# Optimization experiments

Measured on AMD Instinct MI355X. Metric: run time of the kernel, lower is better.

## Reference

```python
import jax, jax.numpy as jnp
import numpy as np

B, T, D, R = 16, 4096, 512, 256

def setup_inputs() -> dict:
    key = jax.random.key(0)
    z = jax.random.normal(key, (B, T, D), dtype=jnp.float32)
    # init values from the module: gegenbauer_weights = [3,0,0], temporal_alpha = -10.0
    gegenbauer_weights = jnp.array([3.0, 0.0, 0.0], dtype=jnp.float32)
    temporal_alpha = jnp.array(-10.0, dtype=jnp.float32)
    # uniformly spaced landmarks, truncated to int like torch.linspace(...).long()
    landmarks = jnp.asarray(np.linspace(0, T - 1, R).astype(np.int64))
    return {"z": z, "gegenbauer_weights": gegenbauer_weights, "temporal_alpha": temporal_alpha, "landmarks": landmarks}

def reference(z, gegenbauer_weights, temporal_alpha, landmarks):
    Bz, Tz, d = z.shape
    # F.normalize(z, dim=-1) with eps=1e-12
    norm = jnp.linalg.norm(z, axis=-1, keepdims=True)
    Q = z / jnp.maximum(norm, 1e-12)
    K = Q[:, landmarks, :]                                   # [B, R, d]
    C = jnp.einsum('btd,brd->btr', Q, K)                     # [B, T, R]
    positions = jnp.arange(Tz)[:, None]                      # [T, 1]
    lm = landmarks[None, :]                                  # [1, R]
    causal_mask = (lm < positions).astype(z.dtype)           # [T, R]
    C_masked = C * causal_mask[None, :, :]
    # Gegenbauer mixture
    alpha = jax.nn.softmax(gegenbauer_weights)
    P1 = (1.0 + C_masked) * 0.5
    P2 = (3.0 * C_masked * C_masked - 1.0) * 0.5
    P3 = (5.0 * C_masked * C_masked * C_masked - 3.0 * C_masked) * 0.5
    Phi = alpha[0] * P1 + alpha[1] * P2 + alpha[2] * P3
    # temporal decay
    temporal_dist = jnp.clip((positions.astype(z.dtype) - lm.astype(z.dtype)) / Tz, 0.0, None)  # [T, R]
    alpha_td = jax.nn.softplus(temporal_alpha)
    Phi = Phi * jnp.exp(-alpha_td * temporal_dist)[None, :, :]
    # rowsum normalize
    row_sum = jnp.maximum(Phi.sum(axis=-1, keepdims=True), 1e-6)
    Phi = Phi / row_sum
    # append constant-1 basis column
    ones = jnp.ones((Bz, Tz, 1), dtype=z.dtype)
    return jnp.concatenate([Phi, ones], axis=-1)             # [B, T, R+1]
```

## Files before the change

kernel.cpp:

```cpp
#include <hip/hip_runtime.h>


typedef float f32x4 __attribute__((ext_vector_type(4)));
typedef short s16x8 __attribute__((ext_vector_type(8)));
typedef unsigned short u16x4 __attribute__((ext_vector_type(4)));
typedef unsigned short u16x8 __attribute__((ext_vector_type(8)));

__device__ __forceinline__ unsigned short f2bf(float f) {
    unsigned u = __builtin_bit_cast(unsigned, f);
    return (unsigned short)((u + 0x7FFFu + ((u >> 16) & 1u)) >> 16);
}

__device__ __forceinline__ int load_lm(const void* lms_raw, int idx) {
    const int* l32 = (const int*)lms_raw;
    if (l32[1] == 0) {
        const long long* l64 = (const long long*)lms_raw;
        return (int)l64[idx];
    }
    return l32[idx];
}

__device__ __forceinline__ void scalars(const float* gw, const float* ta,
                                        float& a0, float& a1, float& a2, float& atd) {
    float w0 = gw[0], w1 = gw[1], w2 = gw[2];
    float wm = fmaxf(w0, fmaxf(w1, w2));
    float e0 = __expf(w0 - wm), e1 = __expf(w1 - wm), e2 = __expf(w2 - wm);
    float einv = 1.0f / (e0 + e1 + e2);
    a0 = e0 * einv; a1 = e1 * einv; a2 = e2 * einv;
    float tv = ta[0];
    atd = (tv > 0.0f) ? (tv + log1pf(__expf(-tv))) : log1pf(__expf(tv));
}

__global__ void build_kt(const float* __restrict__ z,
                         const void* __restrict__ lms_raw,
                         unsigned char* __restrict__ kb) {
    const int b = blockIdx.x >> 8;
    const int r = blockIdx.x & 255;
    const int L = threadIdx.x;
    const int lm = load_lm(lms_raw, r);

    const f32x4* zrow = (const f32x4*)(z + ((size_t)b * 4096 + (size_t)lm) * 512);
    f32x4 v0 = zrow[L * 2 + 0];
    f32x4 v1 = zrow[L * 2 + 1];
    float ss = v0.x*v0.x + v0.y*v0.y + v0.z*v0.z + v0.w*v0.w
             + v1.x*v1.x + v1.y*v1.y + v1.z*v1.z + v1.w*v1.w;
    #pragma unroll
    for (int off = 32; off >= 1; off >>= 1) ss += __shfl_xor(ss, off, 64);
    float inv = 1.0f / fmaxf(sqrtf(ss), 1e-12f);

    u16x8 o;
    o[0]=f2bf(v0.x*inv); o[1]=f2bf(v0.y*inv); o[2]=f2bf(v0.z*inv); o[3]=f2bf(v0.w*inv);
    o[4]=f2bf(v1.x*inv); o[5]=f2bf(v1.y*inv); o[6]=f2bf(v1.z*inv); o[7]=f2bf(v1.w*inv);

    const int w  = r >> 6;
    const int nf = (r >> 4) & 3;
    const int c  = r & 15;
    const int ks = L >> 2;
    const int g  = L & 3;
    size_t off = (size_t)b * 262144 + (size_t)w * 65536
               + (size_t)(ks * 4 + nf) * 1024 + (size_t)(c * 4 + g) * 16;
    *(u16x8*)(kb + off) = o;
}

__global__ __launch_bounds__(256, 4) void nystrom_mfma(const float* __restrict__ z,
                                                       const float* __restrict__ gw,
                                                       const float* __restrict__ ta,
                                                       const void* __restrict__ lms_raw,
                                                       const unsigned char* __restrict__ kb,
                                                       float* __restrict__ out) {
    __shared__ unsigned char qtile[32 * 512 * 2];
    __shared__ float s_invn[32];
    __shared__ float s_rs[4][32];
    __shared__ float s_rsi[32];

    const int tid  = threadIdx.x;
    const int lane = tid & 63;
    const int w    = tid >> 6;
    const int b    = blockIdx.x >> 7;
    const int t0   = (blockIdx.x & 127) * 32;

    const int c = lane & 15;
    const int g = lane >> 4;

    float sa0, sa1, sa2, alpha_td;
    scalars(gw, ta, sa0, sa1, sa2, alpha_td);
    const float C0 = 0.5f * (sa0 - sa1);

    const unsigned char* kbw = kb + (size_t)b * 262144 + (size_t)w * 65536
                             + (size_t)(c * 4 + g) * 16;

    u16x8 bbuf[3][4];
    #pragma unroll
    for (int p = 0; p < 2; ++p)
        #pragma unroll
        for (int nf = 0; nf < 4; ++nf)
            bbuf[p][nf] = *(const u16x8*)(kbw + (p * 4 + nf) * 1024);

    {
        const int row = tid >> 3, part = tid & 7;
        const f32x4* zr = (const f32x4*)(z + ((size_t)b * 4096 + (size_t)(t0 + row)) * 512);
        f32x4 v[16];
        #pragma unroll
        for (int i = 0; i < 16; ++i) v[i] = zr[part + 8 * i];
        float ss = 0.0f;
        #pragma unroll
        for (int i = 0; i < 16; ++i) {
            f32x4 vv = v[i];
            ss += vv.x*vv.x + vv.y*vv.y + vv.z*vv.z + vv.w*vv.w;
            u16x4 h; h[0]=f2bf(vv.x); h[1]=f2bf(vv.y); h[2]=f2bf(vv.z); h[3]=f2bf(vv.w);
            int within = ((part + 8 * i) * 8) ^ ((row & 7) << 4);
            *(u16x4*)(qtile + row * 1024 + within) = h;
        }
        ss += __shfl_xor(ss, 1, 64);
        ss += __shfl_xor(ss, 2, 64);
        ss += __shfl_xor(ss, 4, 64);
        if (part == 0) s_invn[row] = 1.0f / fmaxf(sqrtf(ss), 1e-12f);
    }
    __syncthreads();

    f32x4 acc[2][4];
    #pragma unroll
    for (int tf = 0; tf < 2; ++tf)
        #pragma unroll
        for (int nf = 0; nf < 4; ++nf)
            acc[tf][nf] = 0.0f;

    const int swz = (c & 7) << 4;
    s16x8 abuf[2][2];
    {
        int kw = (0 * 64 + g * 16) ^ swz;
        abuf[0][0] = *(const s16x8*)(qtile + c * 1024 + kw);
        abuf[0][1] = *(const s16x8*)(qtile + (c + 16) * 1024 + kw);
    }

    #pragma unroll
    for (int ks = 0; ks < 16; ++ks) {
        if (ks + 2 < 16) {
            #pragma unroll
            for (int nf = 0; nf < 4; ++nf)
                bbuf[(ks + 2) % 3][nf] =
                    *(const u16x8*)(kbw + ((ks + 2) * 4 + nf) * 1024);
        }
        if (ks + 1 < 16) {
            int kw = ((ks + 1) * 64 + g * 16) ^ swz;
            abuf[(ks + 1) & 1][0] = *(const s16x8*)(qtile + c * 1024 + kw);
            abuf[(ks + 1) & 1][1] = *(const s16x8*)(qtile + (c + 16) * 1024 + kw);
        }
        const s16x8 a0f = abuf[ks & 1][0];
        const s16x8 a1f = abuf[ks & 1][1];
        const s16x8 b0f = __builtin_bit_cast(s16x8, bbuf[ks % 3][0]);
        const s16x8 b1f = __builtin_bit_cast(s16x8, bbuf[ks % 3][1]);
        const s16x8 b2f = __builtin_bit_cast(s16x8, bbuf[ks % 3][2]);
        const s16x8 b3f = __builtin_bit_cast(s16x8, bbuf[ks % 3][3]);
        acc[0][0] = __builtin_amdgcn_mfma_f32_16x16x32_bf16(a0f, b0f, acc[0][0], 0, 0, 0);
        acc[0][1] = __builtin_amdgcn_mfma_f32_16x16x32_bf16(a0f, b1f, acc[0][1], 0, 0, 0);
        acc[0][2] = __builtin_amdgcn_mfma_f32_16x16x32_bf16(a0f, b2f, acc[0][2], 0, 0, 0);
        acc[0][3] = __builtin_amdgcn_mfma_f32_16x16x32_bf16(a0f, b3f, acc[0][3], 0, 0, 0);
        acc[1][0] = __builtin_amdgcn_mfma_f32_16x16x32_bf16(a1f, b0f, acc[1][0], 0, 0, 0);
        acc[1][1] = __builtin_amdgcn_mfma_f32_16x16x32_bf16(a1f, b1f, acc[1][1], 0, 0, 0);
        acc[1][2] = __builtin_amdgcn_mfma_f32_16x16x32_bf16(a1f, b2f, acc[1][2], 0, 0, 0);
        acc[1][3] = __builtin_amdgcn_mfma_f32_16x16x32_bf16(a1f, b3f, acc[1][3], 0, 0, 0);
    }

    int   lmv[4];
    float elm[4];
    #pragma unroll
    for (int nf = 0; nf < 4; ++nf) {
        int rr  = w * 64 + nf * 16 + c;
        lmv[nf] = load_lm(lms_raw, rr);
        elm[nf] = __expf(alpha_td * (float)lmv[nf] * (1.0f / 4096.0f));
    }
    float invn[2][4], et[2][4];
    #pragma unroll
    for (int tf = 0; tf < 2; ++tf)
        #pragma unroll
        for (int q = 0; q < 4; ++q) {
            int tl = tf * 16 + g * 4 + q;
            invn[tf][q] = s_invn[tl];
            et[tf][q]   = __expf(-alpha_td * (float)(t0 + tl) * (1.0f / 4096.0f));
        }

    float phi[2][4][4];
    float rsum[2][4];
    #pragma unroll
    for (int tf = 0; tf < 2; ++tf) {
        #pragma unroll
        for (int q = 0; q < 4; ++q) {
            int tg = t0 + tf * 16 + g * 4 + q;
            float s = 0.0f;
            #pragma unroll
            for (int nf = 0; nf < 4; ++nf) {
                float v = acc[tf][nf][q] * invn[tf][q];
                float p;
                if (lmv[nf] < tg) {
                    float c2 = v * v;
                    float p1 = fmaf(0.5f, v, 0.5f);
                    float p2 = fmaf(1.5f, c2, -0.5f);
                    float p3 = v * fmaf(2.5f, c2, -1.5f);
                    p = (sa0 * p1 + sa1 * p2 + sa2 * p3) * (et[tf][q] * elm[nf]);
                } else {
                    p = C0;
                }
                phi[tf][nf][q] = p;
                s += p;
            }
            rsum[tf][q] = s;
        }
    }

    #pragma unroll
    for (int tf = 0; tf < 2; ++tf)
        #pragma unroll
        for (int q = 0; q < 4; ++q) {
            float s = rsum[tf][q];
            s += __shfl_xor(s, 1, 64);
            s += __shfl_xor(s, 2, 64);
            s += __shfl_xor(s, 4, 64);
            s += __shfl_xor(s, 8, 64);
            rsum[tf][q] = s;
        }
    if (c == 0) {
        #pragma unroll
        for (int tf = 0; tf < 2; ++tf)
            #pragma unroll
            for (int q = 0; q < 4; ++q)
                s_rs[w][tf * 16 + g * 4 + q] = rsum[tf][q];
    }
    __syncthreads();
    if (tid < 32) {
        float s = s_rs[0][tid] + s_rs[1][tid] + s_rs[2][tid] + s_rs[3][tid];
        s_rsi[tid] = 1.0f / fmaxf(s, 1e-6f);
    }
    __syncthreads();

    #pragma unroll
    for (int tf = 0; tf < 2; ++tf)
        #pragma unroll
        for (int q = 0; q < 4; ++q) {
            int tl = tf * 16 + g * 4 + q;
            float ri = s_rsi[tl];
            size_t obase = ((size_t)b * 4096 + (size_t)(t0 + tl)) * 257
                         + (size_t)(w * 64 + c);
            #pragma unroll
            for (int nf = 0; nf < 4; ++nf)
                out[obase + nf * 16] = phi[tf][nf][q] * ri;
        }
    if (tid < 32)
        out[((size_t)b * 4096 + (size_t)(t0 + tid)) * 257 + 256] = 1.0f;
}

extern "C" void kernel_launch(void* const* d_in, const int* in_sizes, int n_in,
                              void* d_out, int out_size, void* d_ws, size_t ws_size,
                              hipStream_t stream) {
    const float* z   = (const float*)d_in[0];
    const float* gw  = (const float*)d_in[1];
    const float* ta  = (const float*)d_in[2];
    const void*  lms = (const void*)d_in[3];
    float* out = (float*)d_out;
    unsigned char* kb = (unsigned char*)d_ws;

    build_kt<<<16 * 256, 64, 0, stream>>>(z, lms, kb);
    nystrom_mfma<<<16 * 128, 256, 0, stream>>>(z, gw, ta, lms, kb, out);
}
```

Before: 68.41 us.

## Enlarge workgroup to 64 rows with 8 waves, retile MFMA and remap blocks

Each workgroup now handles 64 time rows with 512 threads. Each of the 8 waves computes a 64x32 landmark slice instead of a 32x64 one, so the per-wave global reads of the landmark matrix are halved and the Q tile in LDS is reused more. The landmark buffer layout is changed to match, the B-operand prefetch gets one more stage, and the block index is permuted to group work across XCDs. In exchange it uses more LDS per block, which may lower occupancy, and the grid has fewer, larger blocks.

```diff
diff --git a/kernel.cpp b/kernel.cpp
--- a/kernel.cpp
+++ b/kernel.cpp
@@ -52,32 +52,33 @@
     o[0]=f2bf(v0.x*inv); o[1]=f2bf(v0.y*inv); o[2]=f2bf(v0.z*inv); o[3]=f2bf(v0.w*inv);
     o[4]=f2bf(v1.x*inv); o[5]=f2bf(v1.y*inv); o[6]=f2bf(v1.z*inv); o[7]=f2bf(v1.w*inv);
 
-    const int w  = r >> 6;
-    const int nf = (r >> 4) & 3;
+    const int rt = r >> 4;
     const int c  = r & 15;
     const int ks = L >> 2;
     const int g  = L & 3;
-    size_t off = (size_t)b * 262144 + (size_t)w * 65536
-               + (size_t)(ks * 4 + nf) * 1024 + (size_t)(c * 4 + g) * 16;
+    size_t off = (size_t)b * 262144
+               + (size_t)(ks * 16 + rt) * 1024 + (size_t)(c * 4 + g) * 16;
     *(u16x8*)(kb + off) = o;
 }
 
-__global__ __launch_bounds__(256, 4) void nystrom_mfma(const float* __restrict__ z,
+__global__ __launch_bounds__(512, 4) void nystrom_mfma(const float* __restrict__ z,
                                                        const float* __restrict__ gw,
                                                        const float* __restrict__ ta,
                                                        const void* __restrict__ lms_raw,
                                                        const unsigned char* __restrict__ kb,
                                                        float* __restrict__ out) {
-    __shared__ unsigned char qtile[32 * 512 * 2];
-    __shared__ float s_invn[32];
-    __shared__ float s_rs[4][32];
-    __shared__ float s_rsi[32];
+    __shared__ unsigned char qtile[64 * 512 * 2];
+    __shared__ float s_invn[64];
+    __shared__ float s_rs[8][64];
+    __shared__ float s_rsi[64];
 
     const int tid  = threadIdx.x;
     const int lane = tid & 63;
     const int w    = tid >> 6;
-    const int b    = blockIdx.x >> 7;
-    const int t0   = (blockIdx.x & 127) * 32;
+
+    const int wgid = (blockIdx.x & 7) * 128 + (blockIdx.x >> 3);
+    const int b    = wgid >> 6;
+    const int t0   = (wgid & 63) * 64;
 
     const int c = lane & 15;
     const int g = lane >> 4;
@@ -86,15 +87,15 @@
     scalars(gw, ta, sa0, sa1, sa2, alpha_td);
     const float C0 = 0.5f * (sa0 - sa1);
 
-    const unsigned char* kbw = kb + (size_t)b * 262144 + (size_t)w * 65536
-                             + (size_t)(c * 4 + g) * 16;
-
-    u16x8 bbuf[3][4];
-    #pragma unroll
-    for (int p = 0; p < 2; ++p)
-        #pragma unroll
-        for (int nf = 0; nf < 4; ++nf)
-            bbuf[p][nf] = *(const u16x8*)(kbw + (p * 4 + nf) * 1024);
+    const unsigned char* kbw = kb + (size_t)b * 262144 + (size_t)(c * 4 + g) * 16;
+    const int rt0 = 2 * w;
+
+    u16x8 bbuf[4][2];
+    #pragma unroll
+    for (int p = 0; p < 3; ++p)
+        #pragma unroll
+        for (int nf = 0; nf < 2; ++nf)
+            bbuf[p][nf] = *(const u16x8*)(kbw + (size_t)(p * 16 + rt0 + nf) * 1024);
 
     {
         const int row = tid >> 3, part = tid & 7;
@@ -118,61 +119,58 @@
     }
     __syncthreads();
 
-    f32x4 acc[2][4];
-    #pragma unroll
-    for (int tf = 0; tf < 2; ++tf)
-        #pragma unroll
-        for (int nf = 0; nf < 4; ++nf)
+    f32x4 acc[4][2];
+    #pragma unroll
+    for (int tf = 0; tf < 4; ++tf)
+        #pragma unroll
+        for (int nf = 0; nf < 2; ++nf)
             acc[tf][nf] = 0.0f;
 
     const int swz = (c & 7) << 4;
-    s16x8 abuf[2][2];
+    s16x8 abuf[2][4];
     {
         int kw = (0 * 64 + g * 16) ^ swz;
-        abuf[0][0] = *(const s16x8*)(qtile + c * 1024 + kw);
-        abuf[0][1] = *(const s16x8*)(qtile + (c + 16) * 1024 + kw);
+        #pragma unroll
+        for (int tf = 0; tf < 4; ++tf)
+            abuf[0][tf] = *(const s16x8*)(qtile + (c + 16 * tf) * 1024 + kw);
     }
 
     #pragma unroll
     for (int ks = 0; ks < 16; ++ks) {
-        if (ks + 2 < 16) {
-            #pragma unroll
-            for (int nf = 0; nf < 4; ++nf)
-                bbuf[(ks + 2) % 3][nf] =
-                    *(const u16x8*)(kbw + ((ks + 2) * 4 + nf) * 1024);
+        if (ks + 3 < 16) {
+            #pragma unroll
+            for (int nf = 0; nf < 2; ++nf)
+                bbuf[(ks + 3) & 3][nf] =
+                    *(const u16x8*)(kbw + (size_t)((ks + 3) * 16 + rt0 + nf) * 1024);
         }
         if (ks + 1 < 16) {
             int kw = ((ks + 1) * 64 + g * 16) ^ swz;
-            abuf[(ks + 1) & 1][0] = *(const s16x8*)(qtile + c * 1024 + kw);
-            abuf[(ks + 1) & 1][1] = *(const s16x8*)(qtile + (c + 16) * 1024 + kw);
-        }
-        const s16x8 a0f = abuf[ks & 1][0];
-        const s16x8 a1f = abuf[ks & 1][1];
-        const s16x8 b0f = __builtin_bit_cast(s16x8, bbuf[ks % 3][0]);
-        const s16x8 b1f = __builtin_bit_cast(s16x8, bbuf[ks % 3][1]);
-        const s16x8 b2f = __builtin_bit_cast(s16x8, bbuf[ks % 3][2]);
-        const s16x8 b3f = __builtin_bit_cast(s16x8, bbuf[ks % 3][3]);
-        acc[0][0] = __builtin_amdgcn_mfma_f32_16x16x32_bf16(a0f, b0f, acc[0][0], 0, 0, 0);
-        acc[0][1] = __builtin_amdgcn_mfma_f32_16x16x32_bf16(a0f, b1f, acc[0][1], 0, 0, 0);
-        acc[0][2] = __builtin_amdgcn_mfma_f32_16x16x32_bf16(a0f, b2f, acc[0][2], 0, 0, 0);
-        acc[0][3] = __builtin_amdgcn_mfma_f32_16x16x32_bf16(a0f, b3f, acc[0][3], 0, 0, 0);
-        acc[1][0] = __builtin_amdgcn_mfma_f32_16x16x32_bf16(a1f, b0f, acc[1][0], 0, 0, 0);
-        acc[1][1] = __builtin_amdgcn_mfma_f32_16x16x32_bf16(a1f, b1f, acc[1][1], 0, 0, 0);
-        acc[1][2] = __builtin_amdgcn_mfma_f32_16x16x32_bf16(a1f, b2f, acc[1][2], 0, 0, 0);
-        acc[1][3] = __builtin_amdgcn_mfma_f32_16x16x32_bf16(a1f, b3f, acc[1][3], 0, 0, 0);
-    }
-
-    int   lmv[4];
-    float elm[4];
-    #pragma unroll
-    for (int nf = 0; nf < 4; ++nf) {
-        int rr  = w * 64 + nf * 16 + c;
+            #pragma unroll
+            for (int tf = 0; tf < 4; ++tf)
+                abuf[(ks + 1) & 1][tf] =
+                    *(const s16x8*)(qtile + (c + 16 * tf) * 1024 + kw);
+        }
+        const s16x8 b0f = __builtin_bit_cast(s16x8, bbuf[ks & 3][0]);
+        const s16x8 b1f = __builtin_bit_cast(s16x8, bbuf[ks & 3][1]);
+        #pragma unroll
+        for (int tf = 0; tf < 4; ++tf) {
+            const s16x8 af = abuf[ks & 1][tf];
+            acc[tf][0] = __builtin_amdgcn_mfma_f32_16x16x32_bf16(af, b0f, acc[tf][0], 0, 0, 0);
+            acc[tf][1] = __builtin_amdgcn_mfma_f32_16x16x32_bf16(af, b1f, acc[tf][1], 0, 0, 0);
+        }
+    }
+
+    int   lmv[2];
+    float elm[2];
+    #pragma unroll
+    for (int nf = 0; nf < 2; ++nf) {
+        int rr  = 32 * w + nf * 16 + c;
         lmv[nf] = load_lm(lms_raw, rr);
         elm[nf] = __expf(alpha_td * (float)lmv[nf] * (1.0f / 4096.0f));
     }
-    float invn[2][4], et[2][4];
-    #pragma unroll
-    for (int tf = 0; tf < 2; ++tf)
+    float invn[4][4], et[4][4];
+    #pragma unroll
+    for (int tf = 0; tf < 4; ++tf)
         #pragma unroll
         for (int q = 0; q < 4; ++q) {
             int tl = tf * 16 + g * 4 + q;
@@ -180,16 +178,16 @@
             et[tf][q]   = __expf(-alpha_td * (float)(t0 + tl) * (1.0f / 4096.0f));
         }
 
-    float phi[2][4][4];
-    float rsum[2][4];
-    #pragma unroll
-    for (int tf = 0; tf < 2; ++tf) {
+    float phi[4][2][4];
+    float rsum[4][4];
+    #pragma unroll
+    for (int tf = 0; tf < 4; ++tf) {
         #pragma unroll
         for (int q = 0; q < 4; ++q) {
             int tg = t0 + tf * 16 + g * 4 + q;
             float s = 0.0f;
             #pragma unroll
-            for (int nf = 0; nf < 4; ++nf) {
+            for (int nf = 0; nf < 2; ++nf) {
                 float v = acc[tf][nf][q] * invn[tf][q];
                 float p;
                 if (lmv[nf] < tg) {
@@ -209,7 +207,7 @@
     }
 
     #pragma unroll
-    for (int tf = 0; tf < 2; ++tf)
+    for (int tf = 0; tf < 4; ++tf)
         #pragma unroll
         for (int q = 0; q < 4; ++q) {
             float s = rsum[tf][q];
@@ -221,31 +219,33 @@
         }
     if (c == 0) {
         #pragma unroll
-        for (int tf = 0; tf < 2; ++tf)
+        for (int tf = 0; tf < 4; ++tf)
             #pragma unroll
             for (int q = 0; q < 4; ++q)
                 s_rs[w][tf * 16 + g * 4 + q] = rsum[tf][q];
     }
     __syncthreads();
-    if (tid < 32) {
-        float s = s_rs[0][tid] + s_rs[1][tid] + s_rs[2][tid] + s_rs[3][tid];
+    if (tid < 64) {
+        float s = 0.0f;
+        #pragma unroll
+        for (int i = 0; i < 8; ++i) s += s_rs[i][tid];
         s_rsi[tid] = 1.0f / fmaxf(s, 1e-6f);
     }
     __syncthreads();
 
     #pragma unroll
-    for (int tf = 0; tf < 2; ++tf)
+    for (int tf = 0; tf < 4; ++tf)
         #pragma unroll
         for (int q = 0; q < 4; ++q) {
             int tl = tf * 16 + g * 4 + q;
             float ri = s_rsi[tl];
             size_t obase = ((size_t)b * 4096 + (size_t)(t0 + tl)) * 257
-                         + (size_t)(w * 64 + c);
-            #pragma unroll
-            for (int nf = 0; nf < 4; ++nf)
+                         + (size_t)(32 * w + c);
+            #pragma unroll
+            for (int nf = 0; nf < 2; ++nf)
                 out[obase + nf * 16] = phi[tf][nf][q] * ri;
         }
-    if (tid < 32)
+    if (tid < 64)
         out[((size_t)b * 4096 + (size_t)(t0 + tid)) * 257 + 256] = 1.0f;
 }
 
@@ -260,5 +260,5 @@
     unsigned char* kb = (unsigned char*)d_ws;
 
     build_kt<<<16 * 256, 64, 0, stream>>>(z, lms, kb);
-    nystrom_mfma<<<16 * 128, 256, 0, stream>>>(z, gw, ta, lms, kb, out);
-}
+    nystrom_mfma<<<1024, 512, 0, stream>>>(z, gw, ta, lms, kb, out);
+}
```

Result: faster. 60.37 us (-11.7%).
